# Kernel tuning notes

Hardware: AMD Instinct MI355X
Metric: run time of the kernel (lower is better)

The kernel has to match this reference:

```python
import jax, jax.numpy as jnp
import numpy as np

B, SEQ, D_IN = 1, 2048, 2048
NUM_HEADS, DIM_HEAD, NUM_KV = 32, 128, 8
GROUP = NUM_HEADS // NUM_KV
EPS = 1e-6
ROPE_BASE = 1000000.0  # Qwen3 rope theta


def setup_inputs() -> dict:
    key = jax.random.key(0)
    ks = jax.random.split(key, 6)
    x = jax.random.normal(ks[0], (B, SEQ, D_IN), jnp.float32)
    Wq = jax.random.normal(ks[1], (D_IN, NUM_HEADS * DIM_HEAD), jnp.float32) * 0.02
    Wk = jax.random.normal(ks[2], (D_IN, NUM_KV * DIM_HEAD), jnp.float32) * 0.02
    Wv = jax.random.normal(ks[3], (D_IN, NUM_KV * DIM_HEAD), jnp.float32) * 0.02
    Wo = jax.random.normal(ks[4], (NUM_HEADS * DIM_HEAD, D_IN), jnp.float32) * 0.02
    q_scale = jnp.ones((DIM_HEAD,), jnp.float32)
    k_scale = jnp.ones((DIM_HEAD,), jnp.float32)
    # RoPE tables: angles for half dims, duplicated to full head dim (rotate-half convention)
    inv_freq = 1.0 / (ROPE_BASE ** (jnp.arange(0, DIM_HEAD, 2, dtype=jnp.float32) / DIM_HEAD))
    pos = jnp.arange(SEQ, dtype=jnp.float32)
    angles = pos[:, None] * inv_freq[None, :]              # [SEQ, DIM_HEAD//2]
    angles = jnp.concatenate([angles, angles], axis=-1)    # [SEQ, DIM_HEAD]
    cos = jnp.cos(angles)
    sin = jnp.sin(angles)
    mask = jnp.triu(jnp.ones((SEQ, SEQ), dtype=bool), k=1)  # True = masked (causal)
    return {"x": x, "Wq": Wq, "Wk": Wk, "Wv": Wv, "Wo": Wo,
            "q_scale": q_scale, "k_scale": k_scale,
            "cos": cos, "sin": sin, "mask": mask, "start_pos": 0}


def _rmsnorm(h, scale):
    var = jnp.mean(h * h, axis=-1, keepdims=True)
    return h * jax.lax.rsqrt(var + EPS) * scale


def _rope(h, cos, sin, offset):
    # h: [b, heads, n, d]; rotate-half RoPE
    n = h.shape[2]
    c = cos[offset:offset + n][None, None]  # [1,1,n,d]
    s = sin[offset:offset + n][None, None]
    half = h.shape[-1] // 2
    h1, h2 = h[..., :half], h[..., half:]
    rotated = jnp.concatenate([-h2, h1], axis=-1)
    return h * c + rotated * s


def reference(x, Wq, Wk, Wv, Wo, q_scale, k_scale, cos, sin, mask, start_pos):
    b, n, _ = x.shape
    q = (x @ Wq).reshape(b, n, NUM_HEADS, DIM_HEAD).transpose(0, 2, 1, 3)  # [b,H,n,d]
    k = (x @ Wk).reshape(b, n, NUM_KV, DIM_HEAD).transpose(0, 2, 1, 3)     # [b,K,n,d]
    v = (x @ Wv).reshape(b, n, NUM_KV, DIM_HEAD).transpose(0, 2, 1, 3)
    q = _rmsnorm(q, q_scale)
    k = _rmsnorm(k, k_scale)
    q = _rope(q, cos, sin, start_pos)
    k = _rope(k, cos, sin, start_pos)
    # next_cache = (k, v); no prior cache (prefill)
    # GQA: group query heads per kv head instead of repeat_interleave on K/V
    qg = q.reshape(b, NUM_KV, GROUP, n, DIM_HEAD)
    scores = jnp.einsum('bkgqd,bknd->bkgqn', qg, k)
    scores = jnp.where(mask[:n, :n], -jnp.inf, scores)
    weights = jax.nn.softmax(scores / jnp.sqrt(jnp.float32(DIM_HEAD)), axis=-1)
    ctx = jnp.einsum('bkgqn,bknd->bkgqd', weights, v)
    ctx = ctx.reshape(b, NUM_HEADS, n, DIM_HEAD).transpose(0, 2, 1, 3).reshape(b, n, NUM_HEADS * DIM_HEAD)
    out = ctx @ Wo
    return (out, k, v)
```

## Files before the change

### kernel.cpp

```cpp
#include <hip/hip_runtime.h>
#include <hip/hip_bf16.h>
#include <cstdint>

typedef unsigned short u16;
typedef __bf16 bf16x8 __attribute__((ext_vector_type(8)));
typedef float f32x4 __attribute__((ext_vector_type(4)));

#define ASYNC16(g, l)                                                                   \
  __builtin_amdgcn_global_load_lds((__attribute__((address_space(1))) const void*)(g),  \
                                   (__attribute__((address_space(3))) void*)(l), 16, 0, 0)

static __device__ __forceinline__ u16 f2bf(float f) {
  unsigned u = __float_as_uint(f);
  u += 0x7FFFu + ((u >> 16) & 1u);
  return (u16)(u >> 16);
}

static __device__ __forceinline__ float fexp2(float x) {
#if __has_builtin(__builtin_amdgcn_exp2f)
  return __builtin_amdgcn_exp2f(x);
#else
  return exp2f(x);
#endif
}

__global__ __launch_bounds__(256) void cast_bf16(const float* __restrict__ src,
                                                 u16* __restrict__ dst, int n8) {
  int i = blockIdx.x * 256 + threadIdx.x;
  if (i >= n8) return;
  const float4* s4 = (const float4*)src;
  float4 a = s4[2 * (size_t)i], b = s4[2 * (size_t)i + 1];
  u16 r[8] = {f2bf(a.x), f2bf(a.y), f2bf(a.z), f2bf(a.w),
              f2bf(b.x), f2bf(b.y), f2bf(b.z), f2bf(b.w)};
  *(uint4*)(dst + 8 * (size_t)i) = *(uint4*)r;
}

__global__ __launch_bounds__(256) void tcast(const float* __restrict__ src, int ld_src, int col0,
                                             int rows, int cols, u16* __restrict__ dst, int ld_dst) {
  __shared__ float tile[32][33];
  int z = blockIdx.z;
  const float* s = src + col0 + (size_t)z * cols;
  u16* d = dst + (size_t)z * cols * ld_dst;
  int cb = blockIdx.x * 32, rb = blockIdx.y * 32;
  int tx = threadIdx.x, ty = threadIdx.y;
#pragma unroll
  for (int i = 0; i < 4; ++i) {
    int r = rb + ty + i * 8;
    tile[ty + i * 8][tx] = s[(size_t)r * ld_src + cb + tx];
  }
  __syncthreads();
#pragma unroll
  for (int i = 0; i < 4; ++i) {
    int c = cb + ty + i * 8;
    d[(size_t)c * ld_dst + rb + tx] = f2bf(tile[tx][ty + i * 8]);
  }
}

__global__ __launch_bounds__(256) void tcast_v(const float* __restrict__ QKV,
                                               u16* __restrict__ Vt, float* __restrict__ vout) {
  __shared__ float tile[32][33];
  int kv = blockIdx.z;
  const float* s = QKV + 5120 + (size_t)kv * 128;
  u16* d = Vt + (size_t)kv * 128 * 2048;
  float* vo = vout + (size_t)kv * 2048 * 128;
  int cb = blockIdx.x * 32, rb = blockIdx.y * 32;
  int tx = threadIdx.x, ty = threadIdx.y;
#pragma unroll
  for (int i = 0; i < 4; ++i) {
    int r = rb + ty + i * 8;
    float val = s[(size_t)r * 6144 + cb + tx];
    tile[ty + i * 8][tx] = val;
    vo[(size_t)r * 128 + cb + tx] = val;
  }
  __syncthreads();
#pragma unroll
  for (int i = 0; i < 4; ++i) {
    int c = cb + ty + i * 8;
    d[(size_t)c * 2048 + rb + tx] = f2bf(tile[tx][ty + i * 8]);
  }
}

__global__ __launch_bounds__(256) void gemm_bt(const u16* __restrict__ A, const u16* __restrict__ Bt,
                                               float* __restrict__ C, int M, int N, int K) {
  __shared__ char smem[16384];
  char* As = smem;
  char* Bs = smem + 8192;
  const int t = threadIdx.x;
  const int w = t >> 6, l = t & 63, la = l & 15, lh = l >> 4;
  const int wr = w >> 1, wc = w & 1;
  const int m0 = blockIdx.y * 128, n0 = blockIdx.x * 128;
  const u16* Ab = A + (size_t)m0 * K + (size_t)(t >> 2) * K + (t & 3) * 8;
  const u16* Bb = Bt + (size_t)n0 * K + (size_t)(t >> 2) * K + (t & 3) * 8;
  const size_t rowStep = (size_t)64 * K;
  f32x4 acc[4][4];
#pragma unroll
  for (int m = 0; m < 4; ++m)
#pragma unroll
    for (int n = 0; n < 4; ++n) acc[m][n] = (f32x4){0.f, 0.f, 0.f, 0.f};
  char* lA0 = As + w * 1024;
  char* lA1 = As + 4096 + w * 1024;
  char* lB0 = Bs + w * 1024;
  char* lB1 = Bs + 4096 + w * 1024;
  for (int k0 = 0; k0 < K; k0 += 32) {
    __syncthreads();
    ASYNC16(Ab + k0, lA0);
    ASYNC16(Ab + rowStep + k0, lA1);
    ASYNC16(Bb + k0, lB0);
    ASYNC16(Bb + rowStep + k0, lB1);
    __syncthreads();
    bf16x8 af[4], bg[4];
#pragma unroll
    for (int m = 0; m < 4; ++m)
      af[m] = *(const bf16x8*)(As + ((wr * 64 + m * 16 + la) * 32 + lh * 8) * 2);
#pragma unroll
    for (int n = 0; n < 4; ++n)
      bg[n] = *(const bf16x8*)(Bs + ((wc * 64 + n * 16 + la) * 32 + lh * 8) * 2);
#pragma unroll
    for (int m = 0; m < 4; ++m)
#pragma unroll
      for (int n = 0; n < 4; ++n)
        acc[m][n] = __builtin_amdgcn_mfma_f32_16x16x32_bf16(af[m], bg[n], acc[m][n], 0, 0, 0);
  }
#pragma unroll
  for (int m = 0; m < 4; ++m)
#pragma unroll
    for (int n = 0; n < 4; ++n) {
      int row = m0 + wr * 64 + m * 16 + lh * 4;
      int col = n0 + wc * 64 + n * 16 + la;
      float* cp = C + (size_t)row * N + col;
#pragma unroll
      for (int r = 0; r < 4; ++r) cp[(size_t)r * N] = acc[m][n][r];
    }
}

__global__ __launch_bounds__(256) void qk_norm_rope(const float* __restrict__ QKV,
                                                    const float* __restrict__ q_scale,
                                                    const float* __restrict__ k_scale,
                                                    const float* __restrict__ cosT,
                                                    const float* __restrict__ sinT,
                                                    u16* __restrict__ Qb, u16* __restrict__ Kb,
                                                    float* __restrict__ kout) {
  int w = threadIdx.x >> 6, d = threadIdx.x & 63;
  int sidx = blockIdx.x * 4 + w, hi = blockIdx.y;
  bool isQ = hi < 32;
  int col = isQ ? hi * 128 : 4096 + (hi - 32) * 128;
  const float* row = QKV + (size_t)sidx * 6144 + col;
  float v1 = row[d], v2 = row[d + 64];
  float ss = v1 * v1 + v2 * v2;
#pragma unroll
  for (int off = 32; off; off >>= 1) ss += __shfl_xor(ss, off);
  float rn = rsqrtf(ss * (1.0f / 128.0f) + 1e-6f);
  const float* sc = isQ ? q_scale : k_scale;
  float n1 = v1 * rn * sc[d], n2 = v2 * rn * sc[d + 64];
  float c1 = cosT[sidx * 128 + d], s1 = sinT[sidx * 128 + d];
  float c2 = cosT[sidx * 128 + d + 64], s2 = sinT[sidx * 128 + d + 64];
  float o1 = n1 * c1 - n2 * s1;
  float o2 = n2 * c2 + n1 * s2;
  if (isQ) {
    const float qs = 0.12751878878561148f;
    u16* dst = Qb + ((size_t)hi * 2048 + sidx) * 128;
    dst[d] = f2bf(o1 * qs);
    dst[d + 64] = f2bf(o2 * qs);
  } else {
    int kvh = hi - 32;
    u16* dst = Kb + ((size_t)kvh * 2048 + sidx) * 128;
    dst[d] = f2bf(o1);
    dst[d + 64] = f2bf(o2);
    float* fo = kout + ((size_t)kvh * 2048 + sidx) * 128;
    fo[d] = o1;
    fo[d + 64] = o2;
  }
}

__global__ __launch_bounds__(256) void attn(const u16* __restrict__ Q, const u16* __restrict__ Kb,
                                            const u16* __restrict__ Vt, u16* __restrict__ ctx) {
  extern __shared__ char smem[];
  char* Ps = smem + 65536;
  const int t = threadIdx.x, w = t >> 6, l = t & 63, la = l & 15, lh = l >> 4;
  const int bid = blockIdx.x;
  const int g = bid & 7, j_ = bid >> 3;
  const int h = g * 4 + (j_ & 3), p_ = j_ >> 2;
  const int kv = g;
  const int qhA = p_, qhB = 31 - p_;
  const int ntA = qhA + 1, ntT = 33;
  const u16* Kh = Kb + (size_t)kv * 2048 * 128;
  const u16* Vh = Vt + (size_t)kv * 128 * 2048;
  const int keyS = t >> 4, pgK = t & 15;
  const int dS = t >> 3, pgV = t & 7;

  bf16x8 aq[4];
  f32x4 o[8];
  float rmax[4], rsum[4];

  auto loadQ = [&](int q0_) {
    const u16* Qh = Q + ((size_t)h * 2048 + q0_ + w * 16) * 128;
#pragma unroll
    for (int ks = 0; ks < 4; ++ks)
      aq[ks] = *(const bf16x8*)(Qh + la * 128 + ks * 32 + lh * 8);
  };
  auto resetAcc = [&]() {
#pragma unroll
    for (int n = 0; n < 8; ++n) o[n] = (f32x4){0.f, 0.f, 0.f, 0.f};
#pragma unroll
    for (int r = 0; r < 4; ++r) { rmax[r] = -INFINITY; rsum[r] = 0.f; }
  };
  auto STAGE = [&](int buf, int tt) {
    int j0 = (tt >= ntA ? tt - ntA : tt) * 64;
    char* Kd = smem + buf * 32768;
    char* Vd = Kd + 16384;
#pragma unroll
    for (int i = 0; i < 4; ++i) {
      int key = i * 16 + keyS;
      int lg = pgK ^ (key & 7);
      ASYNC16(Kh + (size_t)(j0 + key) * 128 + lg * 8, Kd + i * 4096 + w * 1024);
    }
#pragma unroll
    for (int i = 0; i < 4; ++i) {
      int d = i * 32 + dS;
      int lg = pgV ^ (d & 7);
      ASYNC16(Vh + (size_t)d * 2048 + j0 + lg * 8, Vd + i * 4096 + w * 1024);
    }
  };
  auto epilogue = [&](int q0_) {
#pragma unroll
    for (int r = 0; r < 4; ++r) {
      float inv = 1.f / rsum[r];
      int row = q0_ + w * 16 + lh * 4 + r;
      u16* dst = ctx + (size_t)row * 4096 + h * 128;
#pragma unroll
      for (int n = 0; n < 8; ++n) dst[n * 16 + la] = f2bf(o[n][r] * inv);
    }
  };

  int q0 = qhA * 64;
  loadQ(q0);
  resetAcc();
  STAGE(0, 0);
  asm volatile("s_waitcnt vmcnt(0)" ::: "memory");
  __builtin_amdgcn_s_barrier();
  __builtin_amdgcn_sched_barrier(0);

  int cur = 0;
  for (int tt = 0; tt < ntT; ++tt) {
    if (tt + 1 < ntT) STAGE(cur ^ 1, tt + 1);
    if (tt == ntA) {
      epilogue(q0);
      q0 = qhB * 64;
      loadQ(q0);
      resetAcc();
    }
    const int j0 = (tt >= ntA ? tt - ntA : tt) * 64;
    char* Ks = smem + cur * 32768;
    char* Vs = Ks + 16384;
    f32x4 s[4];
#pragma unroll
    for (int n = 0; n < 4; ++n) s[n] = (f32x4){0.f, 0.f, 0.f, 0.f};
    __builtin_amdgcn_s_setprio(1);
#pragma unroll
    for (int ks = 0; ks < 4; ++ks) {
      bf16x8 bk[4];
#pragma unroll
      for (int n = 0; n < 4; ++n) {
        int key = n * 16 + la;
        int lg = (ks * 4 + lh) ^ (key & 7);
        bk[n] = *(const bf16x8*)(Ks + key * 256 + lg * 16);
      }
#pragma unroll
      for (int n = 0; n < 4; ++n)
        s[n] = __builtin_amdgcn_mfma_f32_16x16x32_bf16(aq[ks], bk[n], s[n], 0, 0, 0);
    }
    __builtin_amdgcn_s_setprio(0);
    {
      int qmin = q0 + w * 16;
#pragma unroll
      for (int n = 0; n < 4; ++n) {
        int jb = j0 + n * 16;
        if (jb + 15 > qmin) {
          int j = jb + la;
#pragma unroll
          for (int r = 0; r < 4; ++r) {
            int q = qmin + lh * 4 + r;
            if (j > q) s[n][r] = -INFINITY;
          }
        }
      }
    }
    float tm[4];
    bool need = false;
#pragma unroll
    for (int r = 0; r < 4; ++r) {
      float v = fmaxf(fmaxf(s[0][r], s[1][r]), fmaxf(s[2][r], s[3][r]));
      v = fmaxf(v, __shfl_xor(v, 1));
      v = fmaxf(v, __shfl_xor(v, 2));
      v = fmaxf(v, __shfl_xor(v, 4));
      v = fmaxf(v, __shfl_xor(v, 8));
      tm[r] = v;
      need |= (v > rmax[r]);
    }
    if (__any(need)) {
#pragma unroll
      for (int r = 0; r < 4; ++r) {
        float nm = fmaxf(rmax[r], tm[r]);
        float fac = fexp2(rmax[r] - nm);
        rmax[r] = nm;
        rsum[r] *= fac;
#pragma unroll
        for (int n = 0; n < 8; ++n) o[n][r] *= fac;
      }
    }
#pragma unroll
    for (int r = 0; r < 4; ++r) {
      float nm = rmax[r];
      float p0 = fexp2(s[0][r] - nm);
      float p1 = fexp2(s[1][r] - nm);
      float p2 = fexp2(s[2][r] - nm);
      float p3 = fexp2(s[3][r] - nm);
      float ps = p0 + p1 + p2 + p3;
      ps += __shfl_xor(ps, 1);
      ps += __shfl_xor(ps, 2);
      ps += __shfl_xor(ps, 4);
      ps += __shfl_xor(ps, 8);
      rsum[r] += ps;
      int qloc = w * 16 + lh * 4 + r;
      int sw = qloc & 7;
      u16 pb[4] = {f2bf(p0), f2bf(p1), f2bf(p2), f2bf(p3)};
#pragma unroll
      for (int n = 0; n < 4; ++n) {
        int key = n * 16 + la;
        *(u16*)(Ps + qloc * 128 + ((key >> 3) ^ sw) * 16 + (key & 7) * 2) = pb[n];
      }
    }
#pragma unroll
    for (int kk = 0; kk < 2; ++kk) {
      bf16x8 ap;
      {
        int qloc = w * 16 + la;
        int lg = (kk * 4 + lh) ^ (qloc & 7);
        ap = *(const bf16x8*)(Ps + qloc * 128 + lg * 16);
      }
      __builtin_amdgcn_s_setprio(1);
#pragma unroll
      for (int n = 0; n < 8; ++n) {
        int d = n * 16 + la;
        int lg = (kk * 4 + lh) ^ (d & 7);
        bf16x8 bv = *(const bf16x8*)(Vs + d * 128 + lg * 16);
        o[n] = __builtin_amdgcn_mfma_f32_16x16x32_bf16(ap, bv, o[n], 0, 0, 0);
      }
      __builtin_amdgcn_s_setprio(0);
    }
    asm volatile("s_waitcnt vmcnt(0)" ::: "memory");
    __builtin_amdgcn_s_barrier();
    __builtin_amdgcn_sched_barrier(0);
    cur ^= 1;
  }
  epilogue(q0);
}

extern "C" void kernel_launch(void* const* d_in, const int* in_sizes, int n_in,
                              void* d_out, int out_size, void* d_ws, size_t ws_size,
                              hipStream_t stream) {
  (void)in_sizes; (void)n_in; (void)out_size; (void)ws_size;
  const float* x = (const float*)d_in[0];
  const float* Wq = (const float*)d_in[1];
  const float* Wk = (const float*)d_in[2];
  const float* Wv = (const float*)d_in[3];
  const float* Wo = (const float*)d_in[4];
  const float* q_scale = (const float*)d_in[5];
  const float* k_scale = (const float*)d_in[6];
  const float* cosT = (const float*)d_in[7];
  const float* sinT = (const float*)d_in[8];
  float* out = (float*)d_out;
  float* kout = out + (size_t)4194304;
  float* vout = out + (size_t)6291456;

  char* p = (char*)d_ws;
  u16* xb = (u16*)p;      p += (size_t)2048 * 2048 * 2;
  u16* WqkvT = (u16*)p;   p += (size_t)6144 * 2048 * 2;
  u16* WoT = (u16*)p;     p += (size_t)2048 * 4096 * 2;
  float* QKV = (float*)p; p += (size_t)2048 * 6144 * 4;
  u16* Qb = (u16*)p;      p += (size_t)32 * 2048 * 128 * 2;
  u16* Kb = (u16*)p;      p += (size_t)8 * 2048 * 128 * 2;
  u16* Vtb = (u16*)p;     p += (size_t)8 * 128 * 2048 * 2;
  u16* ctxb = (u16*)p;    p += (size_t)2048 * 4096 * 2;

  cast_bf16<<<2048, 256, 0, stream>>>(x, xb, 524288);
  tcast<<<dim3(128, 64, 1), dim3(32, 8, 1), 0, stream>>>(Wq, 4096, 0, 2048, 4096, WqkvT, 2048);
  tcast<<<dim3(32, 64, 1), dim3(32, 8, 1), 0, stream>>>(Wk, 1024, 0, 2048, 1024,
                                                        WqkvT + (size_t)4096 * 2048, 2048);
  tcast<<<dim3(32, 64, 1), dim3(32, 8, 1), 0, stream>>>(Wv, 1024, 0, 2048, 1024,
                                                        WqkvT + (size_t)5120 * 2048, 2048);
  tcast<<<dim3(64, 128, 1), dim3(32, 8, 1), 0, stream>>>(Wo, 2048, 0, 4096, 2048, WoT, 4096);
  gemm_bt<<<dim3(48, 16, 1), 256, 0, stream>>>(xb, WqkvT, QKV, 2048, 6144, 2048);
  qk_norm_rope<<<dim3(512, 40, 1), 256, 0, stream>>>(QKV, q_scale, k_scale, cosT, sinT, Qb, Kb, kout);
  tcast_v<<<dim3(4, 64, 8), dim3(32, 8, 1), 0, stream>>>(QKV, Vtb, vout);
  attn<<<dim3(512, 1, 1), 256, 73728, stream>>>(Qb, Kb, Vtb, ctxb);
  gemm_bt<<<dim3(16, 16, 1), 256, 0, stream>>>(ctxb, WoT, out, 2048, 2048, 4096);
}
```

Measured before the change: 451.8 us.

## Double-buffer LDS in GEMM and split-K the output projection

```diff
diff --git a/kernel.cpp b/kernel.cpp
--- a/kernel.cpp
+++ b/kernel.cpp
@@ -82,32 +82,43 @@
 
 __global__ __launch_bounds__(256) void gemm_bt(const u16* __restrict__ A, const u16* __restrict__ Bt,
                                                float* __restrict__ C, int M, int N, int K) {
-  __shared__ char smem[16384];
-  char* As = smem;
-  char* Bs = smem + 8192;
+  __shared__ char smem[32768];
   const int t = threadIdx.x;
   const int w = t >> 6, l = t & 63, la = l & 15, lh = l >> 4;
   const int wr = w >> 1, wc = w & 1;
   const int m0 = blockIdx.y * 128, n0 = blockIdx.x * 128;
-  const u16* Ab = A + (size_t)m0 * K + (size_t)(t >> 2) * K + (t & 3) * 8;
-  const u16* Bb = Bt + (size_t)n0 * K + (size_t)(t >> 2) * K + (t & 3) * 8;
+  const int z = blockIdx.z;
+  const int kLen = K / gridDim.z, kBeg = z * kLen;
+  C += (size_t)z * M * N;
+  const u16* Ab = A + (size_t)m0 * K + (size_t)(t >> 2) * K + (t & 3) * 8 + kBeg;
+  const u16* Bb = Bt + (size_t)n0 * K + (size_t)(t >> 2) * K + (t & 3) * 8 + kBeg;
   const size_t rowStep = (size_t)64 * K;
   f32x4 acc[4][4];
 #pragma unroll
   for (int m = 0; m < 4; ++m)
 #pragma unroll
     for (int n = 0; n < 4; ++n) acc[m][n] = (f32x4){0.f, 0.f, 0.f, 0.f};
-  char* lA0 = As + w * 1024;
-  char* lA1 = As + 4096 + w * 1024;
-  char* lB0 = Bs + w * 1024;
-  char* lB1 = Bs + 4096 + w * 1024;
-  for (int k0 = 0; k0 < K; k0 += 32) {
-    __syncthreads();
-    ASYNC16(Ab + k0, lA0);
-    ASYNC16(Ab + rowStep + k0, lA1);
-    ASYNC16(Bb + k0, lB0);
-    ASYNC16(Bb + rowStep + k0, lB1);
-    __syncthreads();
+
+  auto STAGE = [&](int buf, int k0) {
+    char* As = smem + buf * 16384;
+    char* Bs = As + 8192;
+    ASYNC16(Ab + k0, As + w * 1024);
+    ASYNC16(Ab + rowStep + k0, As + 4096 + w * 1024);
+    ASYNC16(Bb + k0, Bs + w * 1024);
+    ASYNC16(Bb + rowStep + k0, Bs + 4096 + w * 1024);
+  };
+
+  STAGE(0, 0);
+  asm volatile("s_waitcnt vmcnt(0)" ::: "memory");
+  __builtin_amdgcn_s_barrier();
+  __builtin_amdgcn_sched_barrier(0);
+
+  const int nIt = kLen / 32;
+  int buf = 0;
+  for (int it = 0; it < nIt; ++it) {
+    if (it + 1 < nIt) STAGE(buf ^ 1, (it + 1) * 32);
+    char* As = smem + buf * 16384;
+    char* Bs = As + 8192;
     bf16x8 af[4], bg[4];
 #pragma unroll
     for (int m = 0; m < 4; ++m)
@@ -120,6 +131,10 @@
 #pragma unroll
       for (int n = 0; n < 4; ++n)
         acc[m][n] = __builtin_amdgcn_mfma_f32_16x16x32_bf16(af[m], bg[n], acc[m][n], 0, 0, 0);
+    asm volatile("s_waitcnt vmcnt(0)" ::: "memory");
+    __builtin_amdgcn_s_barrier();
+    __builtin_amdgcn_sched_barrier(0);
+    buf ^= 1;
   }
 #pragma unroll
   for (int m = 0; m < 4; ++m)
@@ -131,6 +146,16 @@
 #pragma unroll
       for (int r = 0; r < 4; ++r) cp[(size_t)r * N] = acc[m][n][r];
     }
+}
+
+__global__ __launch_bounds__(256) void addf(const float* __restrict__ a, const float* __restrict__ b,
+                                            float* __restrict__ o, int n4) {
+  int i = blockIdx.x * 256 + threadIdx.x;
+  if (i >= n4) return;
+  float4 x = ((const float4*)a)[i];
+  float4 y = ((const float4*)b)[i];
+  float4 r = {x.x + y.x, x.y + y.y, x.z + y.z, x.w + y.w};
+  ((float4*)o)[i] = r;
 }
 
 __global__ __launch_bounds__(256) void qk_norm_rope(const float* __restrict__ QKV,
@@ -382,6 +407,7 @@
   u16* Kb = (u16*)p;      p += (size_t)8 * 2048 * 128 * 2;
   u16* Vtb = (u16*)p;     p += (size_t)8 * 128 * 2048 * 2;
   u16* ctxb = (u16*)p;    p += (size_t)2048 * 4096 * 2;
+  float* Cp = (float*)d_ws;
 
   cast_bf16<<<2048, 256, 0, stream>>>(x, xb, 524288);
   tcast<<<dim3(128, 64, 1), dim3(32, 8, 1), 0, stream>>>(Wq, 4096, 0, 2048, 4096, WqkvT, 2048);
@@ -394,5 +420,6 @@
   qk_norm_rope<<<dim3(512, 40, 1), 256, 0, stream>>>(QKV, q_scale, k_scale, cosT, sinT, Qb, Kb, kout);
   tcast_v<<<dim3(4, 64, 8), dim3(32, 8, 1), 0, stream>>>(QKV, Vtb, vout);
   attn<<<dim3(512, 1, 1), 256, 73728, stream>>>(Qb, Kb, Vtb, ctxb);
-  gemm_bt<<<dim3(16, 16, 1), 256, 0, stream>>>(ctxb, WoT, out, 2048, 2048, 4096);
-}
+  gemm_bt<<<dim3(16, 16, 2), 256, 0, stream>>>(ctxb, WoT, Cp, 2048, 2048, 4096);
+  addf<<<4096, 256, 0, stream>>>(Cp, Cp + (size_t)4194304, out, 1048576);
+}
```

New measurement: 399.8 us. 1.13x faster.
